# Performance work log

Hardware: AMD Instinct MI355X
Metric: run time of the kernel (lower is better)

## Reference

```python
import jax, jax.numpy as jnp
import numpy as np

N_NODES = 100000
N_EDGES = 3200000
N_GRAPHS = 64


def _seg_mean(vals, idx, num_segments):
    s = jax.ops.segment_sum(vals, idx, num_segments=num_segments)
    cnt = jax.ops.segment_sum(jnp.ones((vals.shape[0],), vals.dtype), idx,
                              num_segments=num_segments)
    return s / jnp.maximum(cnt, 1.0)[:, None]


def _gcn_layer(x, edge_index, edge_attr, Wc, bc, Wn):
    # center = lin1(x)
    center = x @ Wc + bc
    row, col = edge_index[0], edge_index[1]  # row = source (j), col = target (i)
    # degree computed over row indices (as in PyG degree(row))
    deg = jax.ops.segment_sum(jnp.ones((row.shape[0],), x.dtype), row,
                              num_segments=x.shape[0])
    deg_inv_sqrt = jnp.where(deg > 0, jax.lax.rsqrt(jnp.maximum(deg, 1.0)), 0.0)
    norm = deg_inv_sqrt[row] * deg_inv_sqrt[col]  # [E]
    # message: lin2(concat(x_j, edge_attr)) * norm
    msg = jnp.concatenate([x[row], edge_attr], axis=1) @ Wn  # [E, out]
    msg = msg * norm[:, None]
    # aggr='mean' at target nodes
    aggr = _seg_mean(msg, col, x.shape[0])
    return center + aggr


def setup_inputs() -> dict:
    key = jax.random.key(0)
    ks = jax.random.split(key, 12)
    x = jax.random.normal(ks[0], (N_NODES, 3), dtype=jnp.float32)
    edge_index = jax.random.randint(ks[1], (2, N_EDGES), 0, N_NODES, dtype=jnp.int64)
    edge_attr = jax.random.normal(ks[2], (N_EDGES, 2), dtype=jnp.float32)
    batch = jnp.sort(jax.random.randint(ks[3], (N_NODES,), 0, N_GRAPHS, dtype=jnp.int64))
    s = 0.2
    params = {
        'Wc1': jax.random.normal(ks[4], (3, 16), jnp.float32) * s,
        'bc1': jnp.zeros((16,), jnp.float32),
        'Wn1': jax.random.normal(ks[5], (5, 16), jnp.float32) * s,   # in+edge = 3+2
        'Wc2': jax.random.normal(ks[6], (16, 16), jnp.float32) * s,
        'bc2': jnp.zeros((16,), jnp.float32),
        'Wn2': jax.random.normal(ks[7], (18, 16), jnp.float32) * s,  # 16+2
        'Wl1': jax.random.normal(ks[8], (16, 16), jnp.float32) * s,
        'bl1': jnp.zeros((16,), jnp.float32),
        'Wl2': jax.random.normal(ks[9], (16, 2), jnp.float32) * s,
        'bl2': jnp.zeros((2,), jnp.float32),
    }
    return dict(x=x, edge_index=edge_index, edge_attr=edge_attr, batch=batch, **params)


def reference(x, edge_index, edge_attr, batch,
              Wc1, bc1, Wn1, Wc2, bc2, Wn2, Wl1, bl1, Wl2, bl2):
    h = _gcn_layer(x, edge_index, edge_attr, Wc1, bc1, Wn1)
    h = jax.nn.relu(h)  # dropout is identity in eval mode
    h = _gcn_layer(h, edge_index, edge_attr, Wc2, bc2, Wn2)
    h = jax.nn.relu(h)
    g = _seg_mean(h, batch, N_GRAPHS)          # global scatter_mean pooling [G,16]
    g = jax.nn.relu(g @ Wl1 + bl1)
    return g @ Wl2 + bl2                        # [G, 2]
```

## Files before the change

### kernel.cpp

```cpp
#include <hip/hip_runtime.h>

constexpr int TPB  = 256;
constexpr int TPBW = 1024;
constexpr int TPBS = 512;
constexpr int BSH  = 7;
constexpr int BKN  = 128;
constexpr int MAXB = 800;
constexpr int CAP  = 4608;
constexpr int SBUF = 4608;
constexpr int ITER = 9;
constexpr int SIT  = 7;
constexpr int SEDG = SIT * TPBW;
constexpr int HWL  = 12800;

__device__ __forceinline__ unsigned short f2bf(float f) {
    unsigned u = __float_as_uint(f);
    u += 0x7FFFu + ((u >> 16) & 1u);
    return (unsigned short)(u >> 16);
}
__device__ __forceinline__ float bflo(unsigned u) {
    return __uint_as_float(u << 16);
}
__device__ __forceinline__ float bfhi(unsigned u) {
    return __uint_as_float(u & 0xFFFF0000u);
}

__global__ __launch_bounds__(TPBW)
void k_stage2(const int* __restrict__ ei, const float2* __restrict__ ea,
              int E, int NBKT, int W,
              int* __restrict__ gcnt, int2* __restrict__ staged,
              unsigned int* __restrict__ partialR) {
    __shared__ unsigned int lh[HWL];
    __shared__ int cl[MAXB], gb[MAXB];
    const int p = blockIdx.x, t = threadIdx.x;
    for (int i = t; i < W; i += TPBW) lh[i] = 0;
    for (int b = t; b < NBKT; b += TPBW) cl[b] = 0;
    __syncthreads();
    const int* colA = ei + E;
    const int s = p * SEDG, send = min(s + SEDG, E);
    int rid[SIT], eap[SIT], bk[SIT], rk[SIT];
#pragma unroll
    for (int k = 0; k < SIT; k++) {
        int e = s + t + k * TPBW;
        bk[k] = -1;
        if (e < send) {
            int r = ei[e], c = colA[e];
            atomicAdd(&lh[r >> 3], 1u << ((r & 7) * 4));
            int b = c >> BSH;
            float2 ev = ea[e];
            rid[k] = (r << BSH) | (c & (BKN - 1));
            eap[k] = (int)((unsigned)f2bf(ev.x) | ((unsigned)f2bf(ev.y) << 16));
            bk[k] = b;
            rk[k] = atomicAdd(&cl[b], 1);
        }
    }
    __syncthreads();
    for (int b = t; b < NBKT; b += TPBW) {
        int c = cl[b];
        gb[b] = c ? atomicAdd(&gcnt[b], c) : 0;
    }
    __syncthreads();
#pragma unroll
    for (int k = 0; k < SIT; k++) {
        if (bk[k] >= 0) {
            int pos = gb[bk[k]] + rk[k];
            if (pos < CAP)
                staged[(size_t)bk[k] * CAP + pos] = make_int2(rid[k], eap[k]);
        }
    }
    for (int w = t; w < W; w += TPBW) partialR[(size_t)p * W + w] = lh[w];
}

__global__ __launch_bounds__(512)
void k_xd(const unsigned int* __restrict__ partialR, int NP, int W, int N,
          const float* __restrict__ x,
          float* __restrict__ dis, float4* __restrict__ xd) {
    __shared__ unsigned int sA[8][64], sB[8][64];
    const int wloc = threadIdx.x & 63, lane = threadIdx.x >> 6;
    const int w = blockIdx.x * 64 + wloc;
    unsigned int accA = 0, accB = 0;
    if (w < W) {
        for (int p = lane; p < NP; p += 8) {
            unsigned int v = partialR[(size_t)p * W + w];
            accA += v & 0x0F0F0F0Fu;
            accB += (v >> 4) & 0x0F0F0F0Fu;
        }
    }
    sA[lane][wloc] = accA;
    sB[lane][wloc] = accB;
    __syncthreads();
    if (lane == 0 && w < W) {
#pragma unroll
        for (int l = 1; l < 8; l++) { accA += sA[l][wloc]; accB += sB[l][wloc]; }
        int d[8];
        d[0] = accA & 255; d[2] = (accA >> 8) & 255;
        d[4] = (accA >> 16) & 255; d[6] = accA >> 24;
        d[1] = accB & 255; d[3] = (accB >> 8) & 255;
        d[5] = (accB >> 16) & 255; d[7] = accB >> 24;
        const int n0 = w * 8;
#pragma unroll
        for (int k = 0; k < 8; k++) {
            int n = n0 + k;
            if (n < N) {
                float dv = d[k] ? rsqrtf((float)d[k]) : 0.f;
                dis[n] = dv;
                xd[n] = make_float4(x[3 * (size_t)n], x[3 * (size_t)n + 1],
                                    x[3 * (size_t)n + 2], dv);
            }
        }
    }
}

__global__ __launch_bounds__(TPBS)
void k_sortA(int2* __restrict__ staged, const int* __restrict__ gcnt,
             const float4* __restrict__ xd, int N,
             const float* __restrict__ Wc, const float* __restrict__ bc,
             const float* __restrict__ Wn,
             unsigned short* __restrict__ hb, unsigned short* __restrict__ hbs,
             float2* __restrict__ eaS,
             int* __restrict__ cnt, int* __restrict__ base, int* __restrict__ segN) {
    __shared__ int2 sbuf2[SBUF];
    __shared__ int lfill[BKN], lexc[BKN];
    __shared__ float sax[BKN], say[BKN], saz[BKN], se1[BKN], se2[BKN];
    __shared__ float sWc[48], sbc[16], sWn[80];
    __shared__ int stot;
    const int b = blockIdx.x, t = threadIdx.x;
    const size_t s0 = (size_t)b * CAP;
    const int c0 = b << BSH;
    int cb = gcnt[b]; if (cb > CAP) cb = CAP;
    if (t < BKN) lfill[t] = 0;
    if (t < 48) sWc[t] = Wc[t];
    if (t >= 64 && t < 80) sbc[t - 64] = bc[t - 64];
    if (t >= 128 && t < 208) sWn[t - 128] = Wn[t - 128];
    __syncthreads();
    int er[ITER], ep[ITER], rk[ITER];
#pragma unroll
    for (int k = 0; k < ITER; k++) {
        int e = t + k * TPBS;
        rk[k] = -1;
        if (e < cb) {
            int2 v = staged[s0 + e];
            int j = v.x & (BKN - 1);
            er[k] = (int)(((unsigned)v.x) >> BSH);
            ep[k] = v.y;
            rk[k] = atomicAdd(&lfill[j], 1) | (j << 16);
        }
    }
    __syncthreads();
    if (t < 64) {
        int v0 = lfill[2 * t], v1 = lfill[2 * t + 1];
        int sv = v0 + v1, incl = sv;
#pragma unroll
        for (int off = 1; off < 64; off <<= 1) {
            int up = __shfl_up(incl, off, 64);
            if (t >= off) incl += up;
        }
        int exc = incl - sv;
        lexc[2 * t]     = exc;
        lexc[2 * t + 1] = exc + v0;
        if (t == 63) stot = incl;
    }
    __syncthreads();
#pragma unroll
    for (int k = 0; k < ITER; k++) {
        if (rk[k] >= 0) {
            int j = rk[k] >> 16, rr = rk[k] & 0xFFFF;
            sbuf2[lexc[j] + rr] = make_int2(er[k], ep[k]);
        }
    }
    __syncthreads();
    int tot = stot; if (tot > SBUF) tot = SBUF;
    const int grp = t >> 2, sub = t & 3;
    const int node = c0 + grp;
    float a0 = 0.f, a1 = 0.f, a2 = 0.f, b1 = 0.f, b2 = 0.f;
    {
        int e0 = lexc[grp], dg = lfill[grp];
        if (node < N) {
            for (int e = sub; e < dg; e += 4) {
                int2 ve = sbuf2[e0 + e];
                float4 q = xd[ve.x];
                a0 += q.w * q.x;
                a1 += q.w * q.y;
                a2 += q.w * q.z;
                b1 += q.w * bflo((unsigned)ve.y);
                b2 += q.w * bfhi((unsigned)ve.y);
            }
        }
    }
    a0 += __shfl_down(a0, 2, 4); a0 += __shfl_down(a0, 1, 4);
    a1 += __shfl_down(a1, 2, 4); a1 += __shfl_down(a1, 1, 4);
    a2 += __shfl_down(a2, 2, 4); a2 += __shfl_down(a2, 1, 4);
    b1 += __shfl_down(b1, 2, 4); b1 += __shfl_down(b1, 1, 4);
    b2 += __shfl_down(b2, 2, 4); b2 += __shfl_down(b2, 1, 4);
    if (sub == 0) {
        sax[grp] = a0; say[grp] = a1; saz[grp] = a2;
        se1[grp] = b1; se2[grp] = b2;
    }
    {
        int* ridS = (int*)staged;
        for (int i = t; i < tot; i += TPBS) ridS[s0 * 2 + i] = sbuf2[i].x;
    }
    if (t == 0) segN[b] = tot;
    if (t < BKN) {
        int nd = c0 + t;
        if (nd < N) { cnt[nd] = lfill[t]; base[nd] = lexc[t]; }
    }
    __syncthreads();
    if (t < BKN) {
        int nd = c0 + t;
        if (nd < N) {
            float inv = 1.0f / fmaxf((float)lfill[t], 1.0f);
            float4 xq = xd[nd];
            float ldt = xq.w;
            float sc = ldt * inv;
            float m[5] = {sax[t] * sc, say[t] * sc, saz[t] * sc,
                          se1[t] * sc, se2[t] * sc};
            float xv[3] = {xq.x, xq.y, xq.z};
            float o[16];
#pragma unroll
            for (int k = 0; k < 16; k++) {
                float v = sbc[k];
#pragma unroll
                for (int j = 0; j < 3; j++) v += xv[j] * sWc[j * 16 + k];
#pragma unroll
                for (int j = 0; j < 5; j++) v += m[j] * sWn[j * 16 + k];
                o[k] = fmaxf(v, 0.0f);
            }
            unsigned ov[8], sv[8];
#pragma unroll
            for (int q = 0; q < 8; q++) {
                ov[q] = (unsigned)f2bf(o[2 * q]) | ((unsigned)f2bf(o[2 * q + 1]) << 16);
                sv[q] = (unsigned)f2bf(ldt * o[2 * q]) |
                        ((unsigned)f2bf(ldt * o[2 * q + 1]) << 16);
            }
            uint4* hp = (uint4*)(hb + 16 * (size_t)nd);
            hp[0] = make_uint4(ov[0], ov[1], ov[2], ov[3]);
            hp[1] = make_uint4(ov[4], ov[5], ov[6], ov[7]);
            uint4* hps = (uint4*)(hbs + 16 * (size_t)nd);
            hps[0] = make_uint4(sv[0], sv[1], sv[2], sv[3]);
            hps[1] = make_uint4(sv[4], sv[5], sv[6], sv[7]);
            eaS[nd] = make_float2(se1[t] * ldt, se2[t] * ldt);
        }
    }
}

__global__ __launch_bounds__(TPBS)
void k_g2(const int* __restrict__ ridS, const int* __restrict__ cnt,
          const int* __restrict__ base, const int* __restrict__ segN,
          const float* __restrict__ dis, const unsigned short* __restrict__ hb,
          const unsigned short* __restrict__ hbs,
          const float2* __restrict__ eaS, const int* __restrict__ batch, int N,
          const float* __restrict__ Wc, const float* __restrict__ bc,
          const float* __restrict__ Wn,
          float* __restrict__ pool, int* __restrict__ poolcnt) {
    __shared__ int sbuf[SBUF];
    __shared__ int lfill[BKN], lexc[BKN];
    __shared__ float smr[BKN][17];
    __shared__ float sWc[256], sbc[16], sWn[288], sp[1024];
    __shared__ int sc[64];
    const int b = blockIdx.x, t = threadIdx.x;
    const size_t s0 = (size_t)b * CAP * 2;
    const int c0 = b << BSH;
    if (t < BKN) {
        int nd = c0 + t;
        lfill[t] = (nd < N) ? cnt[nd] : 0;
        lexc[t]  = (nd < N) ? base[nd] : 0;
    }
    for (int k = t; k < 256; k += TPBS) sWc[k] = Wc[k];
    for (int k = t; k < 16;  k += TPBS) sbc[k] = bc[k];
    for (int k = t; k < 288; k += TPBS) sWn[k] = Wn[k];
    for (int k = t; k < 1024; k += TPBS) sp[k] = 0.f;
    if (t < 64) sc[t] = 0;
    int tot = segN[b];
    if (tot > SBUF) tot = SBUF;
    for (int i = t; i < tot; i += TPBS) sbuf[i] = ridS[s0 + i];
    __syncthreads();
    const int grp = t >> 2, sub = t & 3;
    const int node = c0 + grp;
    float mm[16];
#pragma unroll
    for (int k = 0; k < 16; k++) mm[k] = 0.f;
    if (node < N) {
        int e0 = lexc[grp], dg = lfill[grp];
        for (int e = sub; e < dg; e += 4) {
            int r = sbuf[e0 + e];
            const uint4* hr = (const uint4*)(hbs + 16 * (size_t)r);
            uint4 A = hr[0], B = hr[1];
            mm[0]  += bflo(A.x);  mm[1]  += bfhi(A.x);
            mm[2]  += bflo(A.y);  mm[3]  += bfhi(A.y);
            mm[4]  += bflo(A.z);  mm[5]  += bfhi(A.z);
            mm[6]  += bflo(A.w);  mm[7]  += bfhi(A.w);
            mm[8]  += bflo(B.x);  mm[9]  += bfhi(B.x);
            mm[10] += bflo(B.y);  mm[11] += bfhi(B.y);
            mm[12] += bflo(B.z);  mm[13] += bfhi(B.z);
            mm[14] += bflo(B.w);  mm[15] += bfhi(B.w);
        }
    }
#pragma unroll
    for (int k = 0; k < 16; k++) {
        mm[k] += __shfl_down(mm[k], 2, 4);
        mm[k] += __shfl_down(mm[k], 1, 4);
    }
    if (sub == 0) {
#pragma unroll
        for (int k = 0; k < 16; k++) smr[grp][k] = mm[k];
    }
    __syncthreads();
    if (t < BKN) {
        int nd = c0 + t;
        if (nd < N) {
            float inv = 1.0f / fmaxf((float)lfill[t], 1.0f);
            float ldt = dis[nd];
            float scm = ldt * inv;
            float m[18];
#pragma unroll
            for (int k = 0; k < 16; k++) m[k] = smr[t][k] * scm;
            float2 es = eaS[nd];
            m[16] = es.x * inv; m[17] = es.y * inv;
            const uint4* hp = (const uint4*)(hb + 16 * (size_t)nd);
            uint4 A = hp[0], B = hp[1];
            float hv[16] = {bflo(A.x), bfhi(A.x), bflo(A.y), bfhi(A.y),
                            bflo(A.z), bfhi(A.z), bflo(A.w), bfhi(A.w),
                            bflo(B.x), bfhi(B.x), bflo(B.y), bfhi(B.y),
                            bflo(B.z), bfhi(B.z), bflo(B.w), bfhi(B.w)};
            int g = batch[nd];
            atomicAdd(&sc[g], 1);
#pragma unroll
            for (int k = 0; k < 16; k++) {
                float v = sbc[k];
#pragma unroll
                for (int j = 0; j < 16; j++) v += hv[j] * sWc[j * 16 + k];
#pragma unroll
                for (int j = 0; j < 18; j++) v += m[j] * sWn[j * 16 + k];
                v = fmaxf(v, 0.0f);
                unsafeAtomicAdd(&sp[g * 16 + k], v);
            }
        }
    }
    __syncthreads();
    for (int k = t; k < 1024; k += TPBS)
        if (sp[k] != 0.0f) unsafeAtomicAdd(&pool[k], sp[k]);
    if (t < 64 && sc[t]) atomicAdd(&poolcnt[t], sc[t]);
}

__global__ void k_final(const float* __restrict__ pool, const int* __restrict__ poolcnt,
                        const float* __restrict__ Wl1, const float* __restrict__ bl1,
                        const float* __restrict__ Wl2, const float* __restrict__ bl2,
                        float* __restrict__ out) {
    int g = threadIdx.x;
    if (g >= 64) return;
    float inv = 1.0f / fmaxf((float)poolcnt[g], 1.0f);
    float gv[16];
#pragma unroll
    for (int k = 0; k < 16; k++) gv[k] = pool[g * 16 + k] * inv;
    float t[16];
#pragma unroll
    for (int k = 0; k < 16; k++) {
        float v = bl1[k];
#pragma unroll
        for (int j = 0; j < 16; j++) v += gv[j] * Wl1[j * 16 + k];
        t[k] = fmaxf(v, 0.0f);
    }
    float o0 = bl2[0], o1 = bl2[1];
#pragma unroll
    for (int j = 0; j < 16; j++) {
        o0 += t[j] * Wl2[j * 2 + 0];
        o1 += t[j] * Wl2[j * 2 + 1];
    }
    out[2 * g + 0] = o0;
    out[2 * g + 1] = o1;
}

extern "C" void kernel_launch(void* const* d_in, const int* in_sizes, int n_in,
                              void* d_out, int out_size, void* d_ws, size_t ws_size,
                              hipStream_t stream) {
    const float* x     = (const float*)d_in[0];
    const int*   ei    = (const int*)  d_in[1];
    const float* ea    = (const float*)d_in[2];
    const int*   batch = (const int*)  d_in[3];
    const float* Wc1   = (const float*)d_in[4];
    const float* bc1   = (const float*)d_in[5];
    const float* Wn1   = (const float*)d_in[6];
    const float* Wc2   = (const float*)d_in[7];
    const float* bc2   = (const float*)d_in[8];
    const float* Wn2   = (const float*)d_in[9];
    const float* Wl1   = (const float*)d_in[10];
    const float* bl1   = (const float*)d_in[11];
    const float* Wl2   = (const float*)d_in[12];
    const float* bl2   = (const float*)d_in[13];
    float* out = (float*)d_out;

    const int N  = in_sizes[0] / 3;
    const int E  = in_sizes[1] / 2;
    const int NBKT = (N + BKN - 1) >> BSH;
    const int SGRID = (E + SEDG - 1) / SEDG;
    const int W = (N + 7) >> 3;

    char* ws = (char*)d_ws;
    size_t o = 0;
    auto alloc = [&](size_t bytes) {
        void* p = ws + o;
        o += (bytes + 255) & ~(size_t)255;
        return p;
    };
    float* pool    = (float*)alloc(64 * 16 * 4);
    int*   poolcnt = (int*)  alloc(64 * 4);
    int*   gcnt    = (int*)  alloc((size_t)NBKT * 4);
    size_t zbytes = o;
    float*  dis     = (float*)alloc((size_t)N * 4);
    float4* xd      = (float4*)alloc((size_t)N * 16);
    float2* eaS     = (float2*)alloc((size_t)N * 8);
    int*    cnt     = (int*)  alloc((size_t)N * 4);
    int*    base    = (int*)  alloc((size_t)N * 4);
    int*    segN    = (int*)  alloc((size_t)NBKT * 4);
    unsigned int* partialR = (unsigned int*)alloc((size_t)SGRID * W * 4);
    int2*   staged  = (int2*)alloc((size_t)NBKT * CAP * 8);
    unsigned short* hb  = (unsigned short*)alloc((size_t)N * 16 * 2);
    unsigned short* hbs = (unsigned short*)alloc((size_t)N * 16 * 2);
    (void)ws_size;

    hipMemsetAsync(d_ws, 0, zbytes, stream);

    k_stage2<<<SGRID, TPBW, 0, stream>>>(ei, (const float2*)ea, E, NBKT, W,
                                         gcnt, staged, partialR);
    k_xd    <<<(W + 63) / 64, 512, 0, stream>>>(partialR, SGRID, W, N, x, dis, xd);
    k_sortA <<<NBKT, TPBS, 0, stream>>>(staged, gcnt, xd, N,
                                        Wc1, bc1, Wn1, hb, hbs, eaS,
                                        cnt, base, segN);
    k_g2    <<<NBKT, TPBS, 0, stream>>>((const int*)staged, cnt, base, segN,
                                        dis, hb, hbs, eaS, batch, N,
                                        Wc2, bc2, Wn2, pool, poolcnt);
    k_final <<<1, 64, 0, stream>>>(pool, poolcnt, Wl1, bl1, Wl2, bl2, out);
}
```

Before: 247.1 us.

## Bucket-sort staged edges in shared memory and widen per-node gather groups

k_stage2 now runs a block-wide prefix scan over bucket counts and sorts edge records into shared memory by bucket. It then writes them to the global staged array in contiguous runs, which should make the global stores coalesced instead of scattered. Separately, the aggregation kernels use 1024 threads with 8 lanes per node instead of 4, adding parallelism per node gather. The cost is a much larger shared-memory footprint in k_stage2, which may limit occupancy, plus the extra synchronization of the log-step scan.

```diff
diff --git a/kernel.cpp b/kernel.cpp
--- a/kernel.cpp
+++ b/kernel.cpp
@@ -2,13 +2,13 @@
 
 constexpr int TPB  = 256;
 constexpr int TPBW = 1024;
-constexpr int TPBS = 512;
+constexpr int TPBS = 1024;
 constexpr int BSH  = 7;
 constexpr int BKN  = 128;
 constexpr int MAXB = 800;
 constexpr int CAP  = 4608;
 constexpr int SBUF = 4608;
-constexpr int ITER = 9;
+constexpr int ITER = 5;
 constexpr int SIT  = 7;
 constexpr int SEDG = SIT * TPBW;
 constexpr int HWL  = 12800;
@@ -31,7 +31,10 @@
               int* __restrict__ gcnt, int2* __restrict__ staged,
               unsigned int* __restrict__ partialR) {
     __shared__ unsigned int lh[HWL];
-    __shared__ int cl[MAXB], gb[MAXB];
+    __shared__ int2 sb2[SEDG];
+    __shared__ unsigned short sbk[SEDG];
+    __shared__ int cl[MAXB], gb[MAXB], rs[MAXB + 1];
+    __shared__ int tmp[1024];
     const int p = blockIdx.x, t = threadIdx.x;
     for (int i = t; i < W; i += TPBW) lh[i] = 0;
     for (int b = t; b < NBKT; b += TPBW) cl[b] = 0;
@@ -55,18 +58,35 @@
         }
     }
     __syncthreads();
+    tmp[t] = (t < NBKT) ? cl[t] : 0;
+    __syncthreads();
+    for (int off = 1; off < 1024; off <<= 1) {
+        int add = (t >= off) ? tmp[t - off] : 0;
+        __syncthreads();
+        tmp[t] += add;
+        __syncthreads();
+    }
+    if (t < NBKT) rs[t] = tmp[t] - cl[t];
+    if (t == NBKT - 1) rs[NBKT] = tmp[t];
+    __syncthreads();
     for (int b = t; b < NBKT; b += TPBW) {
         int c = cl[b];
         gb[b] = c ? atomicAdd(&gcnt[b], c) : 0;
     }
     __syncthreads();
 #pragma unroll
-    for (int k = 0; k < SIT; k++) {
+    for (int k = 0; k < SIT; k++)
         if (bk[k] >= 0) {
-            int pos = gb[bk[k]] + rk[k];
-            if (pos < CAP)
-                staged[(size_t)bk[k] * CAP + pos] = make_int2(rid[k], eap[k]);
-        }
+            int slot = rs[bk[k]] + rk[k];
+            sb2[slot] = make_int2(rid[k], eap[k]);
+            sbk[slot] = (unsigned short)bk[k];
+        }
+    __syncthreads();
+    const int total = rs[NBKT];
+    for (int i = t; i < total; i += TPBW) {
+        int b = sbk[i];
+        int pos = gb[b] + (i - rs[b]);
+        if (pos < CAP) staged[(size_t)b * CAP + pos] = sb2[i];
     }
     for (int w = t; w < W; w += TPBW) partialR[(size_t)p * W + w] = lh[w];
 }
@@ -170,13 +190,13 @@
     }
     __syncthreads();
     int tot = stot; if (tot > SBUF) tot = SBUF;
-    const int grp = t >> 2, sub = t & 3;
+    const int grp = t >> 3, sub = t & 7;
     const int node = c0 + grp;
     float a0 = 0.f, a1 = 0.f, a2 = 0.f, b1 = 0.f, b2 = 0.f;
     {
         int e0 = lexc[grp], dg = lfill[grp];
         if (node < N) {
-            for (int e = sub; e < dg; e += 4) {
+            for (int e = sub; e < dg; e += 8) {
                 int2 ve = sbuf2[e0 + e];
                 float4 q = xd[ve.x];
                 a0 += q.w * q.x;
@@ -187,11 +207,11 @@
             }
         }
     }
-    a0 += __shfl_down(a0, 2, 4); a0 += __shfl_down(a0, 1, 4);
-    a1 += __shfl_down(a1, 2, 4); a1 += __shfl_down(a1, 1, 4);
-    a2 += __shfl_down(a2, 2, 4); a2 += __shfl_down(a2, 1, 4);
-    b1 += __shfl_down(b1, 2, 4); b1 += __shfl_down(b1, 1, 4);
-    b2 += __shfl_down(b2, 2, 4); b2 += __shfl_down(b2, 1, 4);
+    a0 += __shfl_down(a0, 4, 8); a0 += __shfl_down(a0, 2, 8); a0 += __shfl_down(a0, 1, 8);
+    a1 += __shfl_down(a1, 4, 8); a1 += __shfl_down(a1, 2, 8); a1 += __shfl_down(a1, 1, 8);
+    a2 += __shfl_down(a2, 4, 8); a2 += __shfl_down(a2, 2, 8); a2 += __shfl_down(a2, 1, 8);
+    b1 += __shfl_down(b1, 4, 8); b1 += __shfl_down(b1, 2, 8); b1 += __shfl_down(b1, 1, 8);
+    b2 += __shfl_down(b2, 4, 8); b2 += __shfl_down(b2, 2, 8); b2 += __shfl_down(b2, 1, 8);
     if (sub == 0) {
         sax[grp] = a0; say[grp] = a1; saz[grp] = a2;
         se1[grp] = b1; se2[grp] = b2;
@@ -275,14 +295,14 @@
     if (tot > SBUF) tot = SBUF;
     for (int i = t; i < tot; i += TPBS) sbuf[i] = ridS[s0 + i];
     __syncthreads();
-    const int grp = t >> 2, sub = t & 3;
+    const int grp = t >> 3, sub = t & 7;
     const int node = c0 + grp;
     float mm[16];
 #pragma unroll
     for (int k = 0; k < 16; k++) mm[k] = 0.f;
     if (node < N) {
         int e0 = lexc[grp], dg = lfill[grp];
-        for (int e = sub; e < dg; e += 4) {
+        for (int e = sub; e < dg; e += 8) {
             int r = sbuf[e0 + e];
             const uint4* hr = (const uint4*)(hbs + 16 * (size_t)r);
             uint4 A = hr[0], B = hr[1];
@@ -298,8 +318,9 @@
     }
 #pragma unroll
     for (int k = 0; k < 16; k++) {
-        mm[k] += __shfl_down(mm[k], 2, 4);
-        mm[k] += __shfl_down(mm[k], 1, 4);
+        mm[k] += __shfl_down(mm[k], 4, 8);
+        mm[k] += __shfl_down(mm[k], 2, 8);
+        mm[k] += __shfl_down(mm[k], 1, 8);
     }
     if (sub == 0) {
 #pragma unroll
```

Result: slower. 260.9 us (+5.6%).
